# Kernel tuning notes

Measured on AMD Instinct MI355X. Metric: run time of the kernel, lower is better.

The kernel has to match this reference:

```python
import jax, jax.numpy as jnp
import numpy as np


def setup_inputs() -> dict:
    key = jax.random.key(0)
    k1, k2 = jax.random.split(key)
    B, N, M, D = 16, 2048, 2048, 128
    Q = jax.random.normal(k1, (B, N, D), dtype=jnp.float32)
    KV = jax.random.normal(k2, (B, D, M), dtype=jnp.float32)
    log_sigmas = jnp.zeros((1,), dtype=jnp.float32)
    return {"Q": Q, "KV": KV, "log_sigmas": log_sigmas}


def reference(Q, KV, log_sigmas):
    # Q: [B, N, D], KV: [B, D, M]
    # ||q||^2 per row, ||k||^2 per column (norm squared == sum of squares)
    Q_sq = jnp.sum(Q * Q, axis=-1, keepdims=True)        # [B, N, 1]
    KV_sq = jnp.sum(KV * KV, axis=-2, keepdims=True)     # [B, 1, M]
    QKV = jnp.einsum('bnd,bdm->bnm', Q, KV)              # [B, N, M]
    inv_two_sigma_sq = -0.5 / jnp.exp(2.0 * log_sigmas)  # scalar (shape [1])
    # exp(-||q-k||^2 / (2 sigma^2)) fused epilogue
    out = jnp.exp(inv_two_sigma_sq * (Q_sq + KV_sq - 2.0 * QKV))
    return out
```

## Files before the change

kernel.cpp:

```cpp
#include <hip/hip_runtime.h>


#define B_  16
#define N_  2048
#define M_  2048
#define D_  128

typedef _Float16 half8 __attribute__((ext_vector_type(8)));
typedef float    f32x4 __attribute__((ext_vector_type(4)));

__global__ __launch_bounds__(256) void prep_q(const float* __restrict__ Q,
                                              _Float16* __restrict__ Qh,
                                              float* __restrict__ Qsq) {
    const int row  = blockIdx.x * 4 + (threadIdx.x >> 6);
    const int lane = threadIdx.x & 63;
    const float2 v = reinterpret_cast<const float2*>(Q + (size_t)row * D_)[lane];
    float sq = v.x * v.x + v.y * v.y;
    union { _Float16 h[2]; unsigned int u; } pk;
    pk.h[0] = (_Float16)v.x;
    pk.h[1] = (_Float16)v.y;
    reinterpret_cast<unsigned int*>(Qh + (size_t)row * D_)[lane] = pk.u;
    #pragma unroll
    for (int off = 32; off > 0; off >>= 1) sq += __shfl_down(sq, off, 64);
    if (lane == 0) Qsq[row] = sq;
}

__global__ __launch_bounds__(256) void prep_kv(const float* __restrict__ KV,
                                               _Float16* __restrict__ KTh,
                                               float* __restrict__ Ksq) {
    const int b = blockIdx.y;
    const int m = blockIdx.x * 256 + threadIdx.x;
    const float* src = KV + (size_t)b * D_ * M_ + m;
    _Float16*   dst = KTh + ((size_t)b * M_ + m) * D_;
    float sq = 0.f;
    #pragma unroll 2
    for (int k0 = 0; k0 < D_; k0 += 8) {
        union { _Float16 h[8]; int4 v; } buf;
        #pragma unroll
        for (int j = 0; j < 8; ++j) {
            const float v = src[(size_t)(k0 + j) * M_];
            sq += v * v;
            buf.h[j] = (_Float16)v;
        }
        *reinterpret_cast<int4*>(dst + k0) = buf.v;
    }
    Ksq[(size_t)b * M_ + m] = sq;
}

__global__ __launch_bounds__(256) void gauss_gemm(
    const _Float16* __restrict__ Qh, const _Float16* __restrict__ KTh,
    const float* __restrict__ Qsq,  const float* __restrict__ Ksq,
    const float* __restrict__ ls,   float* __restrict__ out) {
    __shared__ _Float16 Ash[128 * 128];
    __shared__ _Float16 Bsh[128 * 128];

    const int b    = blockIdx.y;
    const int bx   = blockIdx.x;
    const int n0   = (bx >> 4) << 7;
    const int m0   = (bx & 15) << 7;
    const int tid  = threadIdx.x;
    const int wave = tid >> 6;
    const int lane = tid & 63;

    const _Float16* Ag = Qh  + ((size_t)b * N_ + n0) * D_;
    const _Float16* Bg = KTh + ((size_t)b * M_ + m0) * D_;

    #pragma unroll
    for (int i = 0; i < 8; ++i) {
        const int off = (wave * 8 + i) * 512;
        __builtin_amdgcn_global_load_lds(
            (const __attribute__((address_space(1))) unsigned int*)(Ag + off + lane * 8),
            (__attribute__((address_space(3))) unsigned int*)(&Ash[off]), 16, 0, 0);
        __builtin_amdgcn_global_load_lds(
            (const __attribute__((address_space(1))) unsigned int*)(Bg + off + lane * 8),
            (__attribute__((address_space(3))) unsigned int*)(&Bsh[off]), 16, 0, 0);
    }
    __syncthreads();

    const int wr = (wave >> 1) * 64;
    const int wc = (wave & 1) * 64;
    const int lm = lane & 15;
    const int lk = (lane >> 4) * 8;

    f32x4 acc[4][4] = {};
    #pragma unroll
    for (int ks = 0; ks < 128; ks += 32) {
        half8 af[4], bf[4];
        #pragma unroll
        for (int r = 0; r < 4; ++r)
            af[r] = *reinterpret_cast<const half8*>(&Ash[(wr + r * 16 + lm) * 128 + ks + lk]);
        #pragma unroll
        for (int c = 0; c < 4; ++c)
            bf[c] = *reinterpret_cast<const half8*>(&Bsh[(wc + c * 16 + lm) * 128 + ks + lk]);
        #pragma unroll
        for (int r = 0; r < 4; ++r)
            #pragma unroll
            for (int c = 0; c < 4; ++c)
                acc[r][c] = __builtin_amdgcn_mfma_f32_16x16x32_f16(af[r], bf[c], acc[r][c], 0, 0, 0);
    }

    const float inv2s = -0.5f * __expf(-2.0f * ls[0]);
    const int l4 = (lane >> 4) * 4;
    const float* qsq = Qsq + (size_t)b * N_ + n0;
    const float* ksq = Ksq + (size_t)b * M_ + m0;
    float* Cb = out + ((size_t)b * N_ + n0) * (size_t)M_ + m0;

    float ksv[4];
    #pragma unroll
    for (int c = 0; c < 4; ++c) ksv[c] = ksq[wc + c * 16 + lm];

    #pragma unroll
    for (int r = 0; r < 4; ++r) {
        #pragma unroll
        for (int i = 0; i < 4; ++i) {
            const int row  = wr + r * 16 + l4 + i;
            const float qv = qsq[row];
            float* Crow = Cb + (size_t)row * M_;
            #pragma unroll
            for (int c = 0; c < 4; ++c) {
                const float t = inv2s * (qv + ksv[c] - 2.0f * acc[r][c][i]);
                Crow[wc + c * 16 + lm] = __expf(t);
            }
        }
    }
}

extern "C" void kernel_launch(void* const* d_in, const int* in_sizes, int n_in,
                              void* d_out, int out_size, void* d_ws, size_t ws_size,
                              hipStream_t stream) {
    const float* Q  = (const float*)d_in[0];
    const float* KV = (const float*)d_in[1];
    const float* ls = (const float*)d_in[2];
    float* out = (float*)d_out;

    char* ws = (char*)d_ws;
    _Float16* Qh  = (_Float16*)ws;
    _Float16* KTh = (_Float16*)(ws + (size_t)8 * 1024 * 1024);
    float*    Qsq = (float*)(ws + (size_t)16 * 1024 * 1024);
    float*    Ksq = (float*)(ws + (size_t)16 * 1024 * 1024 + 128 * 1024);

    prep_q <<<dim3(B_ * N_ / 4), 256, 0, stream>>>(Q, Qh, Qsq);
    prep_kv<<<dim3(M_ / 256, B_), 256, 0, stream>>>(KV, KTh, Ksq);
    gauss_gemm<<<dim3(256, B_), 256, 0, stream>>>(Qh, KTh, Qsq, Ksq, ls, out);
}
```

Before: 319.2 us.

## Swizzle LDS tiles and stage epilogue through shared memory for coalesced stores

Loads the A and B tiles into LDS with an XOR swizzle on 16-byte groups so that the MFMA fragment reads avoid bank conflicts. The epilogue writes the exponentiated tile into a padded shared buffer, then stores it to global memory as fully coalesced 16-byte row writes in place of scattered 4-byte stores. It also hoists the Qsq loads, folds the scaling into an fma, and sets a two-blocks-per-CU launch bound. The cost is an extra LDS round trip and two more barriers, and the larger shared footprint (about 66 KB) may limit how many blocks fit on a CU.

```diff
diff --git a/kernel.cpp b/kernel.cpp
--- a/kernel.cpp
+++ b/kernel.cpp
@@ -47,12 +47,13 @@
     Ksq[(size_t)b * M_ + m] = sq;
 }
 
-__global__ __launch_bounds__(256) void gauss_gemm(
+__global__ __launch_bounds__(256, 2) void gauss_gemm(
     const _Float16* __restrict__ Qh, const _Float16* __restrict__ KTh,
     const float* __restrict__ Qsq,  const float* __restrict__ Ksq,
     const float* __restrict__ ls,   float* __restrict__ out) {
-    __shared__ _Float16 Ash[128 * 128];
-    __shared__ _Float16 Bsh[128 * 128];
+    __shared__ __align__(16) char smem[132 * 128 * 4];
+    _Float16* Ash = (_Float16*)smem;
+    _Float16* Bsh = (_Float16*)(smem + 32768);
 
     const int b    = blockIdx.y;
     const int bx   = blockIdx.x;
@@ -67,31 +68,38 @@
 
     #pragma unroll
     for (int i = 0; i < 8; ++i) {
-        const int off = (wave * 8 + i) * 512;
+        const int chunk = wave * 8 + i;
+        const int r     = chunk * 4 + (lane >> 4);
+        const int g     = (lane & 15) ^ (r & 7);
+        const int goff  = r * 128 + g * 8;
         __builtin_amdgcn_global_load_lds(
-            (const __attribute__((address_space(1))) unsigned int*)(Ag + off + lane * 8),
-            (__attribute__((address_space(3))) unsigned int*)(&Ash[off]), 16, 0, 0);
+            (const __attribute__((address_space(1))) unsigned int*)(Ag + goff),
+            (__attribute__((address_space(3))) unsigned int*)(&Ash[chunk * 512]), 16, 0, 0);
         __builtin_amdgcn_global_load_lds(
-            (const __attribute__((address_space(1))) unsigned int*)(Bg + off + lane * 8),
-            (__attribute__((address_space(3))) unsigned int*)(&Bsh[off]), 16, 0, 0);
+            (const __attribute__((address_space(1))) unsigned int*)(Bg + goff),
+            (__attribute__((address_space(3))) unsigned int*)(&Bsh[chunk * 512]), 16, 0, 0);
     }
     __syncthreads();
 
     const int wr = (wave >> 1) * 64;
     const int wc = (wave & 1) * 64;
     const int lm = lane & 15;
-    const int lk = (lane >> 4) * 8;
+    const int kq = lane >> 4;
+    const int sw = lm & 7;
 
     f32x4 acc[4][4] = {};
     #pragma unroll
     for (int ks = 0; ks < 128; ks += 32) {
+        const int gl = (ks >> 3) + kq;
         half8 af[4], bf[4];
         #pragma unroll
         for (int r = 0; r < 4; ++r)
-            af[r] = *reinterpret_cast<const half8*>(&Ash[(wr + r * 16 + lm) * 128 + ks + lk]);
+            af[r] = *reinterpret_cast<const half8*>(
+                &Ash[(wr + r * 16 + lm) * 128 + ((gl ^ sw) << 3)]);
         #pragma unroll
         for (int c = 0; c < 4; ++c)
-            bf[c] = *reinterpret_cast<const half8*>(&Bsh[(wc + c * 16 + lm) * 128 + ks + lk]);
+            bf[c] = *reinterpret_cast<const half8*>(
+                &Bsh[(wc + c * 16 + lm) * 128 + ((gl ^ sw) << 3)]);
         #pragma unroll
         for (int r = 0; r < 4; ++r)
             #pragma unroll
@@ -100,28 +108,45 @@
     }
 
     const float inv2s = -0.5f * __expf(-2.0f * ls[0]);
+    const float cm2   = -2.0f * inv2s;
     const int l4 = (lane >> 4) * 4;
     const float* qsq = Qsq + (size_t)b * N_ + n0;
     const float* ksq = Ksq + (size_t)b * M_ + m0;
-    float* Cb = out + ((size_t)b * N_ + n0) * (size_t)M_ + m0;
 
     float ksv[4];
     #pragma unroll
     for (int c = 0; c < 4; ++c) ksv[c] = ksq[wc + c * 16 + lm];
+    float qsv[4][4];
+    #pragma unroll
+    for (int r = 0; r < 4; ++r)
+        #pragma unroll
+        for (int i = 0; i < 4; ++i) qsv[r][i] = qsq[wr + r * 16 + l4 + i];
+
+    __syncthreads();
+    float* Csh = (float*)smem;
 
     #pragma unroll
     for (int r = 0; r < 4; ++r) {
         #pragma unroll
         for (int i = 0; i < 4; ++i) {
-            const int row  = wr + r * 16 + l4 + i;
-            const float qv = qsq[row];
-            float* Crow = Cb + (size_t)row * M_;
+            const int row = wr + r * 16 + l4 + i;
             #pragma unroll
             for (int c = 0; c < 4; ++c) {
-                const float t = inv2s * (qv + ksv[c] - 2.0f * acc[r][c][i]);
-                Crow[wc + c * 16 + lm] = __expf(t);
+                const float t = fmaf(cm2, acc[r][c][i], inv2s * (qsv[r][i] + ksv[c]));
+                Csh[row * 132 + wc + c * 16 + lm] = __expf(t);
             }
         }
+    }
+    __syncthreads();
+
+    float* Cb = out + ((size_t)b * N_ + n0) * (size_t)M_ + m0;
+    const int trow = tid >> 5;
+    const int tcol = (tid & 31) << 2;
+    #pragma unroll
+    for (int it = 0; it < 16; ++it) {
+        const int row = it * 8 + trow;
+        const f32x4 v = *reinterpret_cast<const f32x4*>(&Csh[row * 132 + tcol]);
+        *reinterpret_cast<f32x4*>(&Cb[(size_t)row * M_ + tcol]) = v;
     }
 }
 
```

Result: no change. 318.6 us (-0.2%).
